# Kernel tuning notes

Hardware: AMD Instinct MI355X
Metric: run time of the kernel (lower is better)

Reference implementation:

```python
import jax, jax.numpy as jnp
import numpy as np
import math

B = 2
D_MODEL = 2048
L_MAX = 4096
FILTER_ORDER = 64
EMB_DIM = 3
SHORT_K = 3


def setup_inputs() -> dict:
    key = jax.random.key(0)
    ks = jax.random.split(key, 16)
    D = D_MODEL

    def n(k, shape, scale=0.02):
        return jax.random.normal(k, shape, dtype=jnp.float32) * scale

    return {
        "x": jax.random.normal(ks[0], (B, L_MAX, D), dtype=jnp.float32),
        "in_proj_w": n(ks[1], (3 * D, D)),
        "in_proj_b": n(ks[2], (3 * D,)),
        "short_w": n(ks[3], (3 * D, 1, SHORT_K), 0.3),   # depthwise conv weight (O, I/groups=1, K)
        "short_b": n(ks[4], (3 * D,), 0.1),
        "mlp_w0": n(ks[5], (FILTER_ORDER, EMB_DIM), 0.5),
        "mlp_b0": n(ks[6], (FILTER_ORDER,), 0.5),
        "sin_freq": jnp.ones((1, FILTER_ORDER), dtype=jnp.float32),  # Sin module, w=1, shared across MLP layers
        "mlp_w1": n(ks[7], (FILTER_ORDER, FILTER_ORDER), 0.1),
        "mlp_b1": n(ks[8], (FILTER_ORDER,), 0.1),
        "mlp_w2": n(ks[9], (FILTER_ORDER, FILTER_ORDER), 0.1),
        "mlp_b2": n(ks[10], (FILTER_ORDER,), 0.1),
        "mlp_w3": n(ks[11], (D, FILTER_ORDER), 0.1),      # final Linear(order -> d_model, bias=False)
        "filter_bias": jax.random.normal(ks[12], (D,), dtype=jnp.float32),  # HyenaFilter.bias ~ randn
        "out_proj_w": n(ks[13], (D, D)),
        "out_proj_b": n(ks[14], (D,)),
    }


def _pos_emb(L):
    # PositionalEmbedding: t in [0,1], 1 complex band (emb_dim=3 -> bands=1)
    t = jnp.linspace(0.0, 1.0, L)[:, None]               # (L, 1)
    t_resc = jnp.linspace(0.0, L - 1.0, L)
    w = 2.0 * math.pi * t_resc / L                       # (L,)
    bands = (EMB_DIM - 1) // 2
    f = jnp.linspace(1e-4, bands - 1.0, bands)           # (bands,)
    ang = f[None, :] * w[:, None]                        # (L, bands)
    # z = exp(-1j * f * w) -> real = cos, imag = -sin
    z = jnp.concatenate([t, jnp.cos(ang), -jnp.sin(ang)], axis=-1)  # (L, 3)
    return z, t


def _filter_k(L, w0, b0, freq, w1, b1, w2, b2, w3):
    z, t = _pos_emb(L)
    h = jnp.sin(freq * (z @ w0.T + b0))
    h = jnp.sin(freq * (h @ w1.T + b1))
    h = jnp.sin(freq * (h @ w2.T + b2))
    h = h @ w3.T                                         # (L, D)
    # ExponentialModulation: deltas = linspace(log(.01)/1.5, log(.01)/0.3, D)
    max_decay = math.log(0.01) / 0.3
    min_decay = math.log(0.01) / 1.5
    deltas = jnp.linspace(min_decay, max_decay, h.shape[-1])
    decay = jnp.exp(-t * jnp.abs(deltas)[None, :])       # (L, D)
    return (h * decay).T                                 # (D, L)


def _fftconv(u, k, bias):
    # fftconv_ref with gelu=False, no dropout_mask: u (B, D, L), k (D, L), bias (D,)
    L = u.shape[-1]
    n = 2 * L
    k_f = jnp.fft.rfft(k, n=n) / n                       # (D, L+1)
    u_f = jnp.fft.rfft(u, n=n)                           # (B, D, L+1)
    y = jnp.fft.irfft(u_f * k_f, n=n, norm="forward")[..., :L]
    return y + u * bias[:, None]


def reference(x, in_proj_w, in_proj_b, short_w, short_b, mlp_w0, mlp_b0, sin_freq,
              mlp_w1, mlp_b1, mlp_w2, mlp_b2, mlp_w3, filter_bias,
              out_proj_w, out_proj_b):
    Bn, L, D = x.shape
    u = x @ in_proj_w.T + in_proj_b                      # (B, L, 3D)
    u = jnp.transpose(u, (0, 2, 1))                      # (B, 3D, L)
    # depthwise short conv, padding = short_k - 1, truncate to L (causal-ish)
    uc = jax.lax.conv_general_dilated(
        u, short_w, window_strides=(1,),
        padding=[(SHORT_K - 1, SHORT_K - 1)],
        feature_group_count=3 * D,
        dimension_numbers=("NCH", "OIH", "NCH"))
    uc = uc[..., :L] + short_b[None, :, None]
    x0, x1, v = jnp.split(uc, 3, axis=1)                 # each (B, D, L)
    k = _filter_k(L, mlp_w0, mlp_b0, sin_freq, mlp_w1, mlp_b1, mlp_w2, mlp_b2, mlp_w3)
    # order=2 Hyena recurrence: single gated long-conv step
    v = v * x1
    v = _fftconv(v, k, filter_bias)
    y = v * x0                                           # (B, D, L)
    y = jnp.transpose(y, (0, 2, 1))                      # (B, L, D)
    return y @ out_proj_w.T + out_proj_b
```

## Files before the change

kernel.cpp:

```cpp
#include <hip/hip_runtime.h>
#include <hip/hip_bf16.h>
#include <cstdint>
#include <cstddef>

typedef __attribute__((ext_vector_type(8))) short    bf16x8;
typedef __attribute__((ext_vector_type(4))) float    f32x4;
typedef __attribute__((ext_vector_type(8))) unsigned short u16x8;
typedef __attribute__((ext_vector_type(4))) float    f32v4;
typedef __attribute__((ext_vector_type(4))) unsigned short u16v4;

__device__ __forceinline__ float b2f(unsigned short v) {
    return __builtin_bit_cast(float, ((unsigned int)v) << 16);
}
__device__ __forceinline__ unsigned short f2b(float f) {
    unsigned int u = __builtin_bit_cast(unsigned int, f);
    u += 0x7fffu + ((u >> 16) & 1u);
    return (unsigned short)(u >> 16);
}

__device__ __forceinline__ void async16(const void* g, void* l) {
    __builtin_amdgcn_global_load_lds(
        (const __attribute__((address_space(1))) unsigned int*)g,
        (__attribute__((address_space(3))) unsigned int*)l, 16, 0, 0);
}

__global__ __launch_bounds__(256) void cvt_f32_bf16(const float* __restrict__ src,
                                                    unsigned short* __restrict__ dst, int n4) {
    int i = blockIdx.x * blockDim.x + threadIdx.x;
    int stride = gridDim.x * blockDim.x;
    const f32v4* s4 = (const f32v4*)src;
    u16v4* d4 = (u16v4*)dst;
    for (; i < n4; i += stride) {
        f32v4 v = s4[i];
        u16v4 o;
        o.x = f2b(v.x); o.y = f2b(v.y); o.z = f2b(v.z); o.w = f2b(v.w);
        d4[i] = o;
    }
}

template <int MODE>
__global__ __launch_bounds__(256, 2) void gemm_bf16(
    const unsigned short* __restrict__ A,
    const unsigned short* __restrict__ Bw,
    const float* __restrict__ bias,
    void* __restrict__ Cout,
    int M, int N, int K, int Lseq, int CH)
{
    constexpr int SMEM_N = (MODE == 1) ? 16384 : 8192;
    __shared__ unsigned short smem[SMEM_N];

    const int tid  = threadIdx.x;
    const int w    = tid >> 6;
    const int lane = tid & 63;
    const int quad = lane >> 4;
    const int lq   = lane & 15;
    const int n0 = blockIdx.x * 128;
    const int m0 = blockIdx.y * 128;
    const int wave_m = w & 1, wave_n = w >> 1;

    const int rSub = w * 32 + (lane >> 2);
    const int kcol = (lane & 3) * 8;
    const unsigned short* pA0 = A  + (size_t)(m0 + rSub)      * K + kcol;
    const unsigned short* pA1 = A  + (size_t)(m0 + rSub + 16) * K + kcol;
    const unsigned short* pB0 = Bw + (size_t)(n0 + rSub)      * K + kcol;
    const unsigned short* pB1 = Bw + (size_t)(n0 + rSub + 16) * K + kcol;
    char* sb = (char*)smem;
    char* dA0 = sb + w * 2048;
    char* dA1 = sb + w * 2048 + 1024;
    char* dB0 = sb + 8192 + w * 2048;
    char* dB1 = sb + 8192 + w * 2048 + 1024;

    f32x4 acc[4][4] = {};

    const int nIter = K >> 5;
    for (int kt = 0; kt < nIter; ++kt) {
        async16(pA0, dA0); async16(pA1, dA1);
        async16(pB0, dB0); async16(pB1, dB1);
        pA0 += 32; pA1 += 32; pB0 += 32; pB1 += 32;
        __syncthreads();
        bf16x8 af[4], bw[4];
        #pragma unroll
        for (int i = 0; i < 4; ++i) {
            af[i] = *(const bf16x8*)&smem[(wave_m * 64 + i * 16 + lq) * 32 + quad * 8];
            bw[i] = *(const bf16x8*)&smem[4096 + (wave_n * 64 + i * 16 + lq) * 32 + quad * 8];
        }
        #pragma unroll
        for (int i = 0; i < 4; ++i)
            #pragma unroll
            for (int j = 0; j < 4; ++j)
                acc[i][j] = __builtin_amdgcn_mfma_f32_16x16x32_bf16(af[i], bw[j], acc[i][j], 0, 0, 0);
        __syncthreads();
    }

    if (MODE == 0) {
        float* out = (float*)Cout;
        #pragma unroll
        for (int j = 0; j < 4; ++j) {
            const int col = n0 + wave_n * 64 + j * 16 + lq;
            const float bv = bias[col];
            #pragma unroll
            for (int i = 0; i < 4; ++i) {
                const int rowb = m0 + wave_m * 64 + i * 16 + quad * 4;
                f32x4 c = acc[i][j];
                out[(size_t)(rowb + 0) * N + col] = c.x + bv;
                out[(size_t)(rowb + 1) * N + col] = c.y + bv;
                out[(size_t)(rowb + 2) * N + col] = c.z + bv;
                out[(size_t)(rowb + 3) * N + col] = c.w + bv;
            }
        }
    } else {
        #pragma unroll
        for (int j = 0; j < 4; ++j) {
            const int nl = wave_n * 64 + j * 16 + lq;
            const float bv = bias[n0 + nl];
            #pragma unroll
            for (int i = 0; i < 4; ++i) {
                const int ml = wave_m * 64 + i * 16 + quad * 4;
                f32x4 c = acc[i][j];
                smem[nl * 128 + ml + 0] = f2b(c.x + bv);
                smem[nl * 128 + ml + 1] = f2b(c.y + bv);
                smem[nl * 128 + ml + 2] = f2b(c.z + bv);
                smem[nl * 128 + ml + 3] = f2b(c.w + bv);
            }
        }
        __syncthreads();
        unsigned short* uo = (unsigned short*)Cout;
        const int bI = m0 >> 12;
        const int l0 = m0 & 4095;
        for (int e = tid; e < 2048; e += 256) {
            const int nl = e >> 4, seg = e & 15;
            u16x8 v = *(const u16x8*)&smem[nl * 128 + seg * 8];
            *(u16x8*)&uo[(size_t)(bI * CH + n0 + nl) * Lseq + l0 + seg * 8] = v;
        }
    }
}

__global__ __launch_bounds__(256) void filter_kernel(
    const float* __restrict__ w0, const float* __restrict__ b0,
    const float* __restrict__ freq,
    const float* __restrict__ w1, const float* __restrict__ b1,
    const float* __restrict__ w2, const float* __restrict__ b2,
    const float* __restrict__ w3, float* __restrict__ kf)
{
    __shared__ float ha[64][64];
    __shared__ float hb[64][64];
    const int tid = threadIdx.x;
    const int l0 = blockIdx.x * 64;
    const int d0 = blockIdx.y * 256;
    const int l  = tid & 63;
    const int lg = l0 + l;
    const float tt = (float)lg * (1.0f / 4095.0f);
    const float wang = 6.283185307179586f * (float)lg * (1.0f / 4096.0f);
    const float a  = 1e-4f * wang;
    const float z0 = tt, z1 = cosf(a), z2 = -sinf(a);

    for (int e = tid; e < 4096; e += 256) {
        const int dim = e >> 6;
        float pre = z0 * w0[dim * 3] + z1 * w0[dim * 3 + 1] + z2 * w0[dim * 3 + 2] + b0[dim];
        ha[dim][l] = sinf(freq[dim] * pre);
    }
    __syncthreads();
    for (int e = tid; e < 4096; e += 256) {
        const int dim = e >> 6;
        float acc = b1[dim];
        #pragma unroll
        for (int jj = 0; jj < 64; ++jj) acc += w1[dim * 64 + jj] * ha[jj][l];
        hb[dim][l] = sinf(freq[dim] * acc);
    }
    __syncthreads();
    for (int e = tid; e < 4096; e += 256) {
        const int dim = e >> 6;
        float acc = b2[dim];
        #pragma unroll
        for (int jj = 0; jj < 64; ++jj) acc += w2[dim * 64 + jj] * hb[jj][l];
        ha[dim][l] = sinf(freq[dim] * acc);
    }
    __syncthreads();
    for (int d = d0 + (tid >> 6); d < d0 + 256; d += 4) {
        float acc = 0.f;
        #pragma unroll
        for (int jj = 0; jj < 64; ++jj) acc += w3[d * 64 + jj] * ha[jj][l];
        const float delta = fabsf(-3.0701134573253944f + (-5.999245642062483e-3f) * (float)d);
        kf[(size_t)d * 4096 + lg] = acc * __expf(-tt * delta);
    }
}

#define PIDX(i) ((i) + ((i) >> 5))

__device__ __forceinline__ void bfly_f(float& r1, float& i1, float& r2, float& i2, float wr, float wi) {
    float ur = r1, ui = i1, vr = r2, vi = i2;
    r1 = ur + vr; i1 = ui + vi;
    float dr = ur - vr, di = ui - vi;
    r2 = dr * wr - di * wi;
    i2 = dr * wi + di * wr;
}
__device__ __forceinline__ void bfly_i(float& r1, float& i1, float& r2, float& i2, float wr, float wi) {
    float vr = r2 * wr - i2 * wi, vi = r2 * wi + i2 * wr;
    float ur = r1, ui = i1;
    r1 = ur + vr; i1 = ui + vi;
    r2 = ur - vr; i2 = ui - vi;
}

template <int DS, int STR>
__device__ __forceinline__ void fwd_stage(float* re, float* im, int tt) {
    float wr[8], wi[8];
    constexpr float c = -3.14159265358979f / (float)(STR * DS);
    #pragma unroll
    for (int k = 0; k < DS; ++k) __sincosf(c * (float)(tt + STR * k), &wi[k], &wr[k]);
    #pragma unroll
    for (int s = 0; s < 16; ++s)
        if ((s & DS) == 0)
            bfly_f(re[s], im[s], re[s + DS], im[s + DS], wr[s & (DS - 1)], wi[s & (DS - 1)]);
}
template <int DS, int STR>
__device__ __forceinline__ void inv_stage(float* re, float* im, int tt) {
    float wr[8], wi[8];
    constexpr float c = 3.14159265358979f / (float)(STR * DS);
    #pragma unroll
    for (int k = 0; k < DS; ++k) __sincosf(c * (float)(tt + STR * k), &wi[k], &wr[k]);
    #pragma unroll
    for (int s = 0; s < 16; ++s)
        if ((s & DS) == 0)
            bfly_i(re[s], im[s], re[s + DS], im[s + DS], wr[s & (DS - 1)], wi[s & (DS - 1)]);
}

__device__ __forceinline__ void xchg(float* re, float* im, float* fre, float* fim,
                                     int wbase, int wstr, int rbase, int rstr) {
    __syncthreads();
    #pragma unroll
    for (int s = 0; s < 16; ++s) {
        const int i = wbase + wstr * s;
        fre[PIDX(i)] = re[s]; fim[PIDX(i)] = im[s];
    }
    __syncthreads();
    #pragma unroll
    for (int s = 0; s < 16; ++s) {
        const int i = rbase + rstr * s;
        re[s] = fre[PIDX(i)]; im[s] = fim[PIDX(i)];
    }
}

__device__ __forceinline__ void fwd_fft(float* re, float* im, float* fre, float* fim, int t) {
    const int off = t & 31, seg = t >> 5;
    fwd_stage<8, 512>(re, im, t);
    fwd_stage<4, 512>(re, im, t);
    fwd_stage<2, 512>(re, im, t);
    fwd_stage<1, 512>(re, im, t);
    xchg(re, im, fre, fim, t, 512, seg * 512 + off, 32);
    fwd_stage<8, 32>(re, im, off);
    fwd_stage<4, 32>(re, im, off);
    fwd_stage<2, 32>(re, im, off);
    fwd_stage<1, 32>(re, im, off);
    {
        float wr, wi;
        __sincosf(-3.14159265358979f * (float)(off & 15) / 16.0f, &wi, &wr);
        const bool hi = (off & 16) != 0;
        #pragma unroll
        for (int s = 0; s < 16; ++s) {
            float rr = __shfl_xor(re[s], 16);
            float ri = __shfl_xor(im[s], 16);
            if (!hi) { re[s] += rr; im[s] += ri; }
            else {
                float dr = rr - re[s], di = ri - im[s];
                re[s] = dr * wr - di * wi;
                im[s] = dr * wi + di * wr;
            }
        }
    }
    xchg(re, im, fre, fim, seg * 512 + off, 32, 16 * t, 1);
    fwd_stage<8, 1>(re, im, 0);
    fwd_stage<4, 1>(re, im, 0);
    fwd_stage<2, 1>(re, im, 0);
    fwd_stage<1, 1>(re, im, 0);
}

__device__ __forceinline__ void inv_fft(float* re, float* im, float* fre, float* fim, int t) {
    const int off = t & 31, seg = t >> 5;
    inv_stage<1, 1>(re, im, 0);
    inv_stage<2, 1>(re, im, 0);
    inv_stage<4, 1>(re, im, 0);
    inv_stage<8, 1>(re, im, 0);
    xchg(re, im, fre, fim, 16 * t, 1, seg * 512 + off, 32);
    {
        float wr, wi;
        __sincosf(3.14159265358979f * (float)(off & 15) / 16.0f, &wi, &wr);
        const bool hi = (off & 16) != 0;
        #pragma unroll
        for (int s = 0; s < 16; ++s) {
            float rr = __shfl_xor(re[s], 16);
            float ri = __shfl_xor(im[s], 16);
            if (!hi) {
                float vr = rr * wr - ri * wi, vi = rr * wi + ri * wr;
                re[s] += vr; im[s] += vi;
            } else {
                float vr = re[s] * wr - im[s] * wi, vi = re[s] * wi + im[s] * wr;
                re[s] = rr - vr; im[s] = ri - vi;
            }
        }
    }
    inv_stage<1, 32>(re, im, off);
    inv_stage<2, 32>(re, im, off);
    inv_stage<4, 32>(re, im, off);
    inv_stage<8, 32>(re, im, off);
    xchg(re, im, fre, fim, seg * 512 + off, 32, t, 512);
    inv_stage<1, 512>(re, im, t);
    inv_stage<2, 512>(re, im, t);
    inv_stage<4, 512>(re, im, t);
    inv_stage<8, 512>(re, im, t);
}

__global__ __launch_bounds__(512, 1) void hyena_fft_kernel(
    const unsigned short* __restrict__ u,
    const float* __restrict__ kf,
    const float* __restrict__ sw,
    const float* __restrict__ sbv,
    const float* __restrict__ fbias,
    unsigned short* __restrict__ zb)
{
    __shared__ float fre[8448];
    __shared__ float fim[8448];
    __shared__ float ksr[8192];
    __shared__ float ksi[8192];
    const int t = threadIdx.x;
    const int d = blockIdx.x;

    {
        float kr[16], ki[16];
        #pragma unroll
        for (int s = 0; s < 16; ++s) {
            kr[s] = (s < 8) ? kf[(size_t)d * 4096 + t + 512 * s] : 0.f;
            ki[s] = 0.f;
        }
        fwd_fft(kr, ki, fre, fim, t);
        #pragma unroll
        for (int j = 0; j < 16; ++j) { ksr[j * 512 + t] = kr[j]; ksi[j * 512 + t] = ki[j]; }
    }

    const int c0 = d, c1 = 2048 + d, c2 = 4096 + d;
    const float w00 = sw[c0*3+0], w01 = sw[c0*3+1], w02 = sw[c0*3+2], bb0 = sbv[c0];
    const float w10 = sw[c1*3+0], w11 = sw[c1*3+1], w12 = sw[c1*3+2], bb1 = sbv[c1];
    const float w20 = sw[c2*3+0], w21 = sw[c2*3+1], w22 = sw[c2*3+2], bb2 = sbv[c2];
    const float fb = fbias[d];

    float vgr_[2][8], x0r_[2][8];
    float xr[16], xi[16];
    #pragma unroll
    for (int s = 0; s < 8; ++s) {
        const int l = t + (s << 9);
        #pragma unroll
        for (int b = 0; b < 2; ++b) {
            const size_t base = (size_t)b * 6144 * 4096;
            const size_t r0 = base + (size_t)c0 * 4096;
            const size_t r1 = base + (size_t)c1 * 4096;
            const size_t r2 = base + (size_t)c2 * 4096;
            const float a0 = b2f(u[r0 + l]);
            const float a1 = (l >= 1) ? b2f(u[r0 + l - 1]) : 0.f;
            const float a2 = (l >= 2) ? b2f(u[r0 + l - 2]) : 0.f;
            const float x0v = w00 * a2 + w01 * a1 + w02 * a0 + bb0;
            const float e0 = b2f(u[r1 + l]);
            const float e1 = (l >= 1) ? b2f(u[r1 + l - 1]) : 0.f;
            const float e2 = (l >= 2) ? b2f(u[r1 + l - 2]) : 0.f;
            const float x1v = w10 * e2 + w11 * e1 + w12 * e0 + bb1;
            const float g0 = b2f(u[r2 + l]);
            const float g1 = (l >= 1) ? b2f(u[r2 + l - 1]) : 0.f;
            const float g2 = (l >= 2) ? b2f(u[r2 + l - 2]) : 0.f;
            const float vv = w20 * g2 + w21 * g1 + w22 * g0 + bb2;
            const float vg = vv * x1v;
            vgr_[b][s] = vg; x0r_[b][s] = x0v;
            if (b == 0) xr[s] = vg; else xi[s] = vg;
        }
    }
    #pragma unroll
    for (int s = 8; s < 16; ++s) { xr[s] = 0.f; xi[s] = 0.f; }

    fwd_fft(xr, xi, fre, fim, t);
    #pragma unroll
    for (int j = 0; j < 16; ++j) {
        const float krj = ksr[j * 512 + t], kij = ksi[j * 512 + t];
        const float cr = xr[j], ci = xi[j];
        xr[j] = cr * krj - ci * kij;
        xi[j] = cr * kij + ci * krj;
    }
    inv_fft(xr, xi, fre, fim, t);

    const float inv_n = 1.0f / 8192.0f;
    #pragma unroll
    for (int s = 0; s < 8; ++s) {
        const int p = t + (s << 9);
        const float z0 = (xr[s] * inv_n + vgr_[0][s] * fb) * x0r_[0][s];
        const float z1 = (xi[s] * inv_n + vgr_[1][s] * fb) * x0r_[1][s];
        zb[(size_t)d * 4096 + p]          = f2b(z0);
        zb[(size_t)(2048 + d) * 4096 + p] = f2b(z1);
    }
}

__global__ __launch_bounds__(256) void transpose_kernel(const unsigned short* __restrict__ zb,
                                                        unsigned short* __restrict__ zt)
{
    __shared__ unsigned int tile[64][65];
    const int l0 = blockIdx.x * 64, d0 = blockIdx.y * 64, b = blockIdx.z;
    const int tid = threadIdx.x;
    for (int e = tid; e < 4096; e += 256) {
        const int r = e >> 6, c = e & 63;
        tile[r][c] = zb[(size_t)(b * 2048 + d0 + r) * 4096 + l0 + c];
    }
    __syncthreads();
    for (int e = tid; e < 4096; e += 256) {
        const int r = e >> 6, c = e & 63;
        zt[(size_t)(b * 4096 + l0 + r) * 2048 + d0 + c] = (unsigned short)tile[c][r];
    }
}

extern "C" void kernel_launch(void* const* d_in, const int* in_sizes, int n_in,
                              void* d_out, int out_size, void* d_ws, size_t ws_size,
                              hipStream_t stream)
{
    const float* x   = (const float*)d_in[0];
    const float* ipw = (const float*)d_in[1];
    const float* ipb = (const float*)d_in[2];
    const float* sw  = (const float*)d_in[3];
    const float* sb  = (const float*)d_in[4];
    const float* w0  = (const float*)d_in[5];
    const float* b0  = (const float*)d_in[6];
    const float* fr  = (const float*)d_in[7];
    const float* w1  = (const float*)d_in[8];
    const float* b1  = (const float*)d_in[9];
    const float* w2  = (const float*)d_in[10];
    const float* b2  = (const float*)d_in[11];
    const float* w3  = (const float*)d_in[12];
    const float* fb  = (const float*)d_in[13];
    const float* opw = (const float*)d_in[14];
    const float* opb = (const float*)d_in[15];
    float* out = (float*)d_out;

    char* ws = (char*)d_ws;
    unsigned short* xb  = (unsigned short*)ws;
    unsigned short* wbi = xb + 16777216;
    unsigned short* wbo = wbi + 12582912;
    unsigned short* ub  = wbo + 4194304;
    float* kf           = (float*)(ub + 50331648);
    unsigned short* zbm = (unsigned short*)(kf + 8388608);
    unsigned short* ztb = zbm + 16777216;

    cvt_f32_bf16<<<1024, 256, 0, stream>>>(x,   xb,  16777216 / 4);
    cvt_f32_bf16<<<1024, 256, 0, stream>>>(ipw, wbi, 12582912 / 4);
    cvt_f32_bf16<<<512,  256, 0, stream>>>(opw, wbo, 4194304 / 4);

    gemm_bf16<1><<<dim3(48, 64), 256, 0, stream>>>(xb, wbi, ipb, ub, 8192, 6144, 2048, 4096, 6144);

    filter_kernel<<<dim3(64, 8), 256, 0, stream>>>(w0, b0, fr, w1, b1, w2, b2, w3, kf);

    hyena_fft_kernel<<<2048, 512, 0, stream>>>(ub, kf, sw, sb, fb, zbm);

    transpose_kernel<<<dim3(64, 32, 2), 256, 0, stream>>>(zbm, ztb);

    gemm_bf16<0><<<dim3(16, 64), 256, 0, stream>>>(ztb, wbo, opb, out, 8192, 2048, 2048, 4096, 2048);
}
```

Before: 894.5 us.

## Split filter FFT into separate kernel to cut LDS and raise occupancy

Moves the forward FFT of the long-conv filter out of the main Hyena FFT kernel into its own kernel, which writes the filter spectrum to global memory as interleaved float4. The main kernel drops its two 32KB LDS spectrum buffers and its launch bound goes from 1 to 4 blocks per CU, so more blocks can be resident and latency hidden. It also reloads the spectrum from global memory per channel and adds a launch. The workspace is re-aliased so buffers share memory, and the output-weight conversion now runs after the transpose.

```diff
diff --git a/kernel.cpp b/kernel.cpp
--- a/kernel.cpp
+++ b/kernel.cpp
@@ -309,9 +309,34 @@
     inv_stage<8, 512>(re, im, t);
 }
 
-__global__ __launch_bounds__(512, 1) void hyena_fft_kernel(
+__global__ __launch_bounds__(512, 4) void kfft_kernel(
+    const float* __restrict__ kf,
+    float* __restrict__ kspec)
+{
+    __shared__ float fre[8448];
+    __shared__ float fim[8448];
+    const int t = threadIdx.x;
+    const int d = blockIdx.x;
+    float kr[16], ki[16];
+    #pragma unroll
+    for (int s = 0; s < 16; ++s) {
+        kr[s] = (s < 8) ? kf[(size_t)d * 4096 + t + 512 * s] : 0.f;
+        ki[s] = 0.f;
+    }
+    fwd_fft(kr, ki, fre, fim, t);
+    f32x4* kv = (f32x4*)kspec + (size_t)d * 4096 + t;
+    #pragma unroll
+    for (int q = 0; q < 8; ++q) {
+        f32x4 o;
+        o.x = kr[2 * q]; o.y = ki[2 * q];
+        o.z = kr[2 * q + 1]; o.w = ki[2 * q + 1];
+        kv[q * 512] = o;
+    }
+}
+
+__global__ __launch_bounds__(512, 4) void hyena_fft_kernel(
     const unsigned short* __restrict__ u,
-    const float* __restrict__ kf,
+    const float* __restrict__ kspec,
     const float* __restrict__ sw,
     const float* __restrict__ sbv,
     const float* __restrict__ fbias,
@@ -319,22 +344,8 @@
 {
     __shared__ float fre[8448];
     __shared__ float fim[8448];
-    __shared__ float ksr[8192];
-    __shared__ float ksi[8192];
     const int t = threadIdx.x;
     const int d = blockIdx.x;
-
-    {
-        float kr[16], ki[16];
-        #pragma unroll
-        for (int s = 0; s < 16; ++s) {
-            kr[s] = (s < 8) ? kf[(size_t)d * 4096 + t + 512 * s] : 0.f;
-            ki[s] = 0.f;
-        }
-        fwd_fft(kr, ki, fre, fim, t);
-        #pragma unroll
-        for (int j = 0; j < 16; ++j) { ksr[j * 512 + t] = kr[j]; ksi[j * 512 + t] = ki[j]; }
-    }
 
     const int c0 = d, c1 = 2048 + d, c2 = 4096 + d;
     const float w00 = sw[c0*3+0], w01 = sw[c0*3+1], w02 = sw[c0*3+2], bb0 = sbv[c0];
@@ -374,12 +385,20 @@
     for (int s = 8; s < 16; ++s) { xr[s] = 0.f; xi[s] = 0.f; }
 
     fwd_fft(xr, xi, fre, fim, t);
-    #pragma unroll
-    for (int j = 0; j < 16; ++j) {
-        const float krj = ksr[j * 512 + t], kij = ksi[j * 512 + t];
-        const float cr = xr[j], ci = xi[j];
-        xr[j] = cr * krj - ci * kij;
-        xi[j] = cr * kij + ci * krj;
+    {
+        const f32x4* kv = (const f32x4*)kspec + (size_t)d * 4096 + t;
+        f32x4 kk[8];
+        #pragma unroll
+        for (int q = 0; q < 8; ++q) kk[q] = kv[q * 512];
+        #pragma unroll
+        for (int q = 0; q < 8; ++q) {
+            float cr = xr[2 * q], ci = xi[2 * q];
+            xr[2 * q] = cr * kk[q].x - ci * kk[q].y;
+            xi[2 * q] = cr * kk[q].y + ci * kk[q].x;
+            cr = xr[2 * q + 1]; ci = xi[2 * q + 1];
+            xr[2 * q + 1] = cr * kk[q].z - ci * kk[q].w;
+            xi[2 * q + 1] = cr * kk[q].w + ci * kk[q].z;
+        }
     }
     inv_fft(xr, xi, fre, fim, t);
 
@@ -434,25 +453,29 @@
     float* out = (float*)d_out;
 
     char* ws = (char*)d_ws;
-    unsigned short* xb  = (unsigned short*)ws;
-    unsigned short* wbi = xb + 16777216;
-    unsigned short* wbo = wbi + 12582912;
-    unsigned short* ub  = wbo + 4194304;
-    float* kf           = (float*)(ub + 50331648);
-    unsigned short* zbm = (unsigned short*)(kf + 8388608);
-    unsigned short* ztb = zbm + 16777216;
+    unsigned short* xb    = (unsigned short*)ws;
+    unsigned short* wbi   = (unsigned short*)(ws + 33554432);
+    float*          kspec = (float*)ws;
+    unsigned short* ztb   = (unsigned short*)ws;
+    unsigned short* wbo   = (unsigned short*)(ws + 33554432);
+    unsigned short* ub    = (unsigned short*)(ws + 134217728);
+    float*          kf    = (float*)(ws + 234881024);
+    unsigned short* zbm   = (unsigned short*)(ws + 234881024);
 
     cvt_f32_bf16<<<1024, 256, 0, stream>>>(x,   xb,  16777216 / 4);
     cvt_f32_bf16<<<1024, 256, 0, stream>>>(ipw, wbi, 12582912 / 4);
+
+    gemm_bf16<1><<<dim3(48, 64), 256, 0, stream>>>(xb, wbi, ipb, ub, 8192, 6144, 2048, 4096, 6144);
+
+    filter_kernel<<<dim3(64, 8), 256, 0, stream>>>(w0, b0, fr, w1, b1, w2, b2, w3, kf);
+
+    kfft_kernel<<<2048, 512, 0, stream>>>(kf, kspec);
+
+    hyena_fft_kernel<<<2048, 512, 0, stream>>>(ub, kspec, sw, sb, fb, zbm);
+
+    transpose_kernel<<<dim3(64, 32, 2), 256, 0, stream>>>(zbm, ztb);
+
     cvt_f32_bf16<<<512,  256, 0, stream>>>(opw, wbo, 4194304 / 4);
 
-    gemm_bf16<1><<<dim3(48, 64), 256, 0, stream>>>(xb, wbi, ipb, ub, 8192, 6144, 2048, 4096, 6144);
-
-    filter_kernel<<<dim3(64, 8), 256, 0, stream>>>(w0, b0, fr, w1, b1, w2, b2, w3, kf);
-
-    hyena_fft_kernel<<<2048, 512, 0, stream>>>(ub, kf, sw, sb, fb, zbm);
-
-    transpose_kernel<<<dim3(64, 32, 2), 256, 0, stream>>>(zbm, ztb);
-
     gemm_bf16<0><<<dim3(16, 64), 256, 0, stream>>>(ztb, wbo, opb, out, 8192, 2048, 2048, 4096, 2048);
 }
```

After: 945.1 us. 5.6% more time.
